# Performance work log

Measured on AMD Instinct MI355X. Metric: run time of the kernel, lower is better.

Reference implementation:

```python
import jax, jax.numpy as jnp
import numpy as np

NS = 4  # ns_mesh hard-coded to [4,4,4] in the original forward


def _interp_weights(positions, cell):
    """Order-3 (M3) B-spline interpolation weights and periodic mesh indices.

    Returns w27 (N,27) combined weights and lin (N,27) flat mesh indices.
    """
    frac = positions @ jnp.linalg.inv(cell)          # fractional coords (N,3)
    u = frac * NS
    nearest = jnp.floor(u + 0.5)
    x = u - nearest                                   # in [-0.5, 0.5]
    # order-3 assignment weights at offsets -1, 0, +1
    w = jnp.stack([0.5 * (0.5 - x) ** 2,
                   0.75 - x ** 2,
                   0.5 * (0.5 + x) ** 2], axis=-1)    # (N,3dims,3offs)
    offs = jnp.array([-1, 0, 1], dtype=jnp.int32)
    idx = (nearest[..., None].astype(jnp.int32) + offs) % NS  # (N,3,3)
    w27 = (w[:, 0, :, None, None] * w[:, 1, None, :, None] * w[:, 2, None, None, :]
           ).reshape(-1, 27)
    lin = (idx[:, 0, :, None, None] * NS * NS
           + idx[:, 1, None, :, None] * NS
           + idx[:, 2, None, None, :]).reshape(-1, 27)
    return w27, lin


def _kspace_filter(cell, sigma2):
    """Smeared-Coulomb kernel exp(-k^2 sigma2/2)/k^2 on the rfft half-grid."""
    G = 2.0 * jnp.pi * jnp.linalg.inv(cell).T         # reciprocal lattice rows
    fx = jnp.fft.fftfreq(NS) * NS                     # integer frequencies
    fz = jnp.fft.rfftfreq(NS) * NS
    kvec = (fx[:, None, None, None] * G[0]
            + fx[None, :, None, None] * G[1]
            + fz[None, None, :, None] * G[2])         # (NS,NS,NS//2+1,3)
    k2 = jnp.sum(kvec ** 2, axis=-1)
    k2_safe = jnp.where(k2 > 0, k2, 1.0)
    return jnp.where(k2 > 0, jnp.exp(-k2 * sigma2 * 0.5) / k2_safe, 0.0)


def reference(positions, cell, charges, sigma2, W1, b1, W2, b2, W3, b3):
    w27, lin = _interp_weights(positions, cell)       # (N,27) each
    C = charges.shape[1]
    # points_to_mesh: scatter-add charges with stencil weights
    contrib = (w27[:, :, None] * charges[:, None, :]).reshape(-1, C)
    mesh_flat = jnp.zeros((NS ** 3, C), charges.dtype).at[lin.reshape(-1)].add(contrib)
    mesh = mesh_flat.T.reshape(C, NS, NS, NS)
    # k-space filter: rfft (backward norm) -> multiply -> irfft (forward norm)
    kernel = _kspace_filter(cell, sigma2)
    mesh_hat = jnp.fft.rfftn(mesh, axes=(1, 2, 3))
    mesh = jnp.fft.irfftn(mesh_hat * kernel, s=(NS, NS, NS), axes=(1, 2, 3),
                          norm="forward")
    # mesh_to_points: gather with the same stencil weights
    mesh_flat = mesh.reshape(C, -1).T                 # (NS^3, C)
    pot = jnp.sum(mesh_flat[lin] * w27[:, :, None], axis=1)  # (N,C)
    # tiny MLP on [charge, potential]
    x = jnp.concatenate([charges, pot], axis=1)       # (N,2)
    x = jnp.tanh(x @ W1 + b1)
    x = jnp.tanh(x @ W2 + b2)
    return jnp.sum(x @ W3 + b3)


def setup_inputs() -> dict:
    key = jax.random.key(0)
    ks = jax.random.split(key, 8)
    N = 2_000_000
    L = 6.0
    positions = jax.random.uniform(ks[0], (N, 3), dtype=jnp.float32) * L
    cell = jnp.eye(3, dtype=jnp.float32) * L
    charges = jax.random.normal(ks[1], (N, 1), dtype=jnp.float32)
    sigma2 = jnp.asarray(1.0, dtype=jnp.float32)
    s1, s2, s3 = (1.0 / np.sqrt(2), 1.0 / np.sqrt(10), 1.0 / np.sqrt(10))
    W1 = jax.random.normal(ks[2], (2, 10), jnp.float32) * s1
    b1 = jnp.zeros((10,), jnp.float32)
    W2 = jax.random.normal(ks[3], (10, 10), jnp.float32) * s2
    b2 = jnp.zeros((10,), jnp.float32)
    W3 = jax.random.normal(ks[4], (10, 1), jnp.float32) * s3
    b3 = jnp.zeros((1,), jnp.float32)
    return {"positions": positions, "cell": cell, "charges": charges,
            "sigma2": sigma2, "W1": W1, "b1": b1, "W2": W2, "b2": b2,
            "W3": W3, "b3": b3}
```

## Files before the change

### kernel.cpp

```cpp
#include <hip/hip_runtime.h>
#include <math.h>

#define NSM 4
#define NCELL 64
#define R1_BLOCKS 64

typedef float f32x2 __attribute__((ext_vector_type(2)));


__device__ __forceinline__ f32x2 splat2(float s) { f32x2 v; v.x = s; v.y = s; return v; }

__device__ __forceinline__ f32x2 pkfma(f32x2 a, f32x2 b, f32x2 c) {
#if __has_builtin(__builtin_elementwise_fma)
    return __builtin_elementwise_fma(a, b, c);
#else
    f32x2 r; r.x = fmaf(a.x, b.x, c.x); r.y = fmaf(a.y, b.y, c.y); return r;
#endif
}

__device__ __forceinline__ void inv3x3(const float* __restrict__ C, float* inv) {
    float a=C[0],b=C[1],c=C[2],d=C[3],e=C[4],f=C[5],g=C[6],h=C[7],i=C[8];
    float A  =  (e*i - f*h);
    float B  = -(d*i - f*g);
    float Cc =  (d*h - e*g);
    float det = a*A + b*B + c*Cc;
    float rd = 1.0f/det;
    inv[0] = A*rd;        inv[1] = (c*h - b*i)*rd; inv[2] = (b*f - c*e)*rd;
    inv[3] = B*rd;        inv[4] = (a*i - c*g)*rd; inv[5] = (c*d - a*f)*rd;
    inv[6] = Cc*rd;       inv[7] = (b*g - a*h)*rd; inv[8] = (a*e - b*d)*rd;
}

struct AxW { float wm, w0, wp; int n; };
__device__ __forceinline__ AxW axw(float u) {
    AxW r;
    float nf = rintf(u);
    float x  = u - nf;
    r.w0 = 0.75f - x*x;
    float tm = 0.5f - x;  r.wm = 0.5f*tm*tm;
    float tp = 0.5f + x;  r.wp = 0.5f*tp*tp;
    r.n = ((int)nf) & 3;
    return r;
}

__device__ __forceinline__ void axis_w4(float u, float* __restrict__ W) {
    AxW a = axw(u);
    #pragma unroll
    for (int j = 0; j < 4; j++) {
        float w = (a.n == j)         ? a.w0 : 0.0f;
        w       = (a.n == ((j+1)&3)) ? a.wm : w;
        w       = (a.n == ((j+3)&3)) ? a.wp : w;
        W[j] = w;
    }
}

__device__ __forceinline__ float tanh1(float x) {
    float e = __expf(x + x);
    return fmaf(-2.0f, __builtin_amdgcn_rcpf(e + 1.0f), 1.0f);
}
__device__ __forceinline__ f32x2 tanh2v(f32x2 v) {
    float e0 = __expf(v.x + v.x);
    float e1 = __expf(v.y + v.y);
    f32x2 r;
    r.x = fmaf(-2.0f, __builtin_amdgcn_rcpf(e0 + 1.0f), 1.0f);
    r.y = fmaf(-2.0f, __builtin_amdgcn_rcpf(e1 + 1.0f), 1.0f);
    return r;
}


__device__ __forceinline__ void scatter_one(float px, float py, float pz, float q,
                                            const float* __restrict__ ci,
                                            f32x2* __restrict__ macc) {
    float fx = px*ci[0] + py*ci[3] + pz*ci[6];
    float fy = px*ci[1] + py*ci[4] + pz*ci[7];
    float fz = px*ci[2] + py*ci[5] + pz*ci[8];
    float X[4], Y[4], Z[4];
    axis_w4(fx*(float)NSM, X);
    axis_w4(fy*(float)NSM, Y);
    axis_w4(fz*(float)NSM, Z);
    f32x2 z01; z01.x = Z[0]; z01.y = Z[1];
    f32x2 z23; z23.x = Z[2]; z23.y = Z[3];
    float qX[4];
    #pragma unroll
    for (int x = 0; x < 4; x++) qX[x] = q * X[x];
    #pragma unroll
    for (int x = 0; x < 4; x++) {
        #pragma unroll
        for (int y = 0; y < 4; y++) {
            f32x2 w2 = splat2(qX[x] * Y[y]);
            macc[x*8 + y*2    ] = pkfma(w2, z01, macc[x*8 + y*2    ]);
            macc[x*8 + y*2 + 1] = pkfma(w2, z23, macc[x*8 + y*2 + 1]);
        }
    }
}

__global__ __launch_bounds__(256) void scatter_kernel(
        const float* __restrict__ pos, const float* __restrict__ cell,
        const float* __restrict__ charges, float* __restrict__ partial, int N) {
    __shared__ f32x2 red[128][32];
    __shared__ f32x2 red2[8][32];
    float ci[9]; inv3x3(cell, ci);

    f32x2 macc[32];
    #pragma unroll
    for (int c = 0; c < 32; c++) macc[c] = splat2(0.0f);

    const float4* posv = (const float4*)pos;
    const float4* qv   = (const float4*)charges;
    long b = (long)blockIdx.x * blockDim.x + threadIdx.x;
    long i = b * 4;
    if (i + 3 < N) {
        float4 p0 = posv[3*b], p1 = posv[3*b+1], p2 = posv[3*b+2];
        float4 q4 = qv[b];
        scatter_one(p0.x, p0.y, p0.z, q4.x, ci, macc);
        scatter_one(p0.w, p1.x, p1.y, q4.y, ci, macc);
        scatter_one(p1.z, p1.w, p2.x, q4.z, ci, macc);
        scatter_one(p2.y, p2.z, p2.w, q4.w, ci, macc);
    } else if (i < N) {
        for (long k = i; k < N; k++)
            scatter_one(pos[3*k], pos[3*k+1], pos[3*k+2], charges[k], ci, macc);
    }

    #pragma unroll
    for (int c = 0; c < 32; c++) {
        macc[c].x += __shfl_xor(macc[c].x, 32);
        macc[c].y += __shfl_xor(macc[c].y, 32);
    }
    int t = threadIdx.x;
    int row = (t >> 6) * 32 + (t & 31);
    if ((t & 32) == 0) {
        int sw = t & 31;
        #pragma unroll
        for (int c = 0; c < 32; c++) red[row][c ^ sw] = macc[c];
    }
    __syncthreads();
    int p = t & 31, g = t >> 5;
    f32x2 sum = splat2(0.0f);
    #pragma unroll
    for (int i2 = 0; i2 < 16; i2++) {
        int r = g*16 + i2;
        sum += red[r][p ^ (r & 31)];
    }
    red2[g][p] = sum;
    __syncthreads();
    if (t < NCELL) {
        const float* r2 = (const float*)&red2[0][0];
        int pair = t >> 1, comp = t & 1;
        float s = 0.0f;
        #pragma unroll
        for (int gg = 0; gg < 8; gg++) s += r2[(gg*32 + pair)*2 + comp];
        partial[(long)blockIdx.x * NCELL + t] = s;
    }
}


__global__ __launch_bounds__(256) void reduce_stage1_kernel(
        const float* __restrict__ partial, int nb, float* __restrict__ partial2) {
    __shared__ float acc[4][64];
    int t = threadIdx.x;
    int c = t & 63, g = t >> 6;
    float s = 0.0f;
    for (int r = blockIdx.x + 64*g; r < nb; r += 256)
        s += partial[(long)r * NCELL + c];
    acc[g][c] = s;
    __syncthreads();
    if (t < 64) {
        float v = ((acc[0][t] + acc[1][t]) + acc[2][t]) + acc[3][t];
        partial2[(long)blockIdx.x * NCELL + t] = v;
    }
}


__global__ __launch_bounds__(256) void reduce_filter_kernel(
        const float* __restrict__ partial2,
        const float* __restrict__ cell, const float* __restrict__ sigma2p,
        float* __restrict__ mesh_out) {
    __shared__ float4 redA[16][16];
    __shared__ float mm[64];
    __shared__ float gr[64];
    int t = threadIdx.x;

    int c4 = t & 15, g = t >> 4;
    float4 v = make_float4(0.f, 0.f, 0.f, 0.f);
    const float4* p4 = (const float4*)partial2;
    for (int b = g; b < R1_BLOCKS; b += 16) {
        float4 x = p4[b*16 + c4];
        v.x += x.x; v.y += x.y; v.z += x.z; v.w += x.w;
    }
    redA[g][c4] = v;
    __syncthreads();
    if (t < 16) {
        float4 tot = make_float4(0.f, 0.f, 0.f, 0.f);
        #pragma unroll
        for (int gg = 0; gg < 16; gg++) {
            float4 x = redA[gg][t];
            tot.x += x.x; tot.y += x.y; tot.z += x.z; tot.w += x.w;
        }
        ((float4*)mm)[t] = tot;
    }
    __syncthreads();

    if (t < 64) {
        float ci[9]; inv3x3(cell, ci);
        float s2 = sigma2p[0];
        const float twopi = 6.2831853071795864769f;
        float G0x = twopi*ci[0], G0y = twopi*ci[3], G0z = twopi*ci[6];
        float G1x = twopi*ci[1], G1y = twopi*ci[4], G1z = twopi*ci[7];
        float G2x = twopi*ci[2], G2y = twopi*ci[5], G2z = twopi*ci[8];
        int dx = t >> 4, dy = (t >> 2) & 3, dz = t & 3;
        float acc = 0.0f;
        for (int a = 0; a < 4; a++) {
            float fa = (a < 2) ? (float)a : (float)(a - 4);
            for (int b = 0; b < 4; b++) {
                float fb = (b < 2) ? (float)b : (float)(b - 4);
                for (int c = 0; c < 4; c++) {
                    if ((a | b | c) == 0) continue;
                    float fc = (c < 2) ? (float)c : (float)(c - 4);
                    float kx = fa*G0x + fb*G1x + fc*G2x;
                    float ky = fa*G0y + fb*G1y + fc*G2y;
                    float kz = fa*G0z + fb*G1z + fc*G2z;
                    float k2 = kx*kx + ky*ky + kz*kz;
                    float K  = expf(-k2 * s2 * 0.5f) / k2;
                    int ph = (a*dx + b*dy + c*dz) & 3;
                    float cs = (ph == 0) ? 1.0f : ((ph == 2) ? -1.0f : 0.0f);
                    acc += K * cs;
                }
            }
        }
        gr[t] = acc;
    }
    __syncthreads();
    if (t < 64) {
        int dx = t >> 4, dy = (t >> 2) & 3, dz = t & 3;
        float o = 0.0f;
        for (int s = 0; s < 64; s++) {
            int sx = s >> 4, sy = (s >> 2) & 3, sz = s & 3;
            int d = ((dx - sx) & 3)*16 + ((dy - sy) & 3)*4 + ((dz - sz) & 3);
            o += gr[d] * mm[s];
        }
        mesh_out[t] = o;
    }
}


__device__ __forceinline__ float pot_one(float px, float py, float pz,
                                         const float* __restrict__ ci,
                                         const float* __restrict__ mpad) {
    float fx = px*ci[0] + py*ci[3] + pz*ci[6];
    float fy = px*ci[1] + py*ci[4] + pz*ci[7];
    float fz = px*ci[2] + py*ci[5] + pz*ci[8];
    AxW X = axw(fx*(float)NSM);
    AxW Y = axw(fy*(float)NSM);
    AxW Z = axw(fz*(float)NSM);
    int base = X.n*36 + Y.n*6 + Z.n;
    float yacc[3];
    #pragma unroll
    for (int a = 0; a < 3; a++) {
        float zc0, zc1, zc2;
        {
            const float* r = &mpad[base + a*36];
            zc0 = Z.wm*r[0];  zc0 = fmaf(Z.w0, r[1], zc0);  zc0 = fmaf(Z.wp, r[2], zc0);
            zc1 = Z.wm*r[6];  zc1 = fmaf(Z.w0, r[7], zc1);  zc1 = fmaf(Z.wp, r[8], zc1);
            zc2 = Z.wm*r[12]; zc2 = fmaf(Z.w0, r[13], zc2); zc2 = fmaf(Z.wp, r[14], zc2);
        }
        float s = Y.wm*zc0;
        s = fmaf(Y.w0, zc1, s);
        s = fmaf(Y.wp, zc2, s);
        yacc[a] = s;
    }
    float pot = X.wm*yacc[0];
    pot = fmaf(X.w0, yacc[1], pot);
    pot = fmaf(X.wp, yacc[2], pot);
    return pot;
}

__global__ __launch_bounds__(256) void gather_mlp_kernel(
        const float* __restrict__ pos, const float* __restrict__ cell,
        const float* __restrict__ charges,
        const float* __restrict__ W1, const float* __restrict__ b1,
        const float* __restrict__ W2, const float* __restrict__ b2,
        const float* __restrict__ W3, const float* __restrict__ b3,
        const float* __restrict__ meshf, float* __restrict__ bsum, int N) {
    __shared__ float mpad[216];
    __shared__ float wavesum[4];
    if (threadIdx.x < 216) {
        int i = threadIdx.x / 36, rem = threadIdx.x % 36;
        int j = rem / 6, k = rem % 6;
        mpad[threadIdx.x] = meshf[((i+3)&3)*16 + ((j+3)&3)*4 + ((k+3)&3)];
    }
    float ci[9]; inv3x3(cell, ci);

    float w1r0[10], w1r1[10], b1r[10], w2r[10][10], b2r[10], w3r[10];
    #pragma unroll
    for (int j = 0; j < 10; j++) {
        w1r0[j] = W1[j]; w1r1[j] = W1[10 + j];
        b1r[j] = b1[j];  b2r[j] = b2[j]; w3r[j] = W3[j];
    }
    #pragma unroll
    for (int i = 0; i < 10; i++) {
        #pragma unroll
        for (int j = 0; j < 10; j++) w2r[i][j] = W2[10*i + j];
    }
    float b3r = b3[0];
    __syncthreads();

    long t4 = (long)blockIdx.x * blockDim.x + threadIdx.x;
    long i0 = t4 * 4;
    float ysum = 0.0f;

    if (i0 + 3 < N) {
        const float4* posv = (const float4*)pos;
        float4 p0 = posv[3*t4], p1 = posv[3*t4+1], p2 = posv[3*t4+2];
        float4 q4 = ((const float4*)charges)[t4];

        float pt0 = pot_one(p0.x, p0.y, p0.z, ci, mpad);
        float pt1 = pot_one(p0.w, p1.x, p1.y, ci, mpad);
        float pt2 = pot_one(p1.z, p1.w, p2.x, ci, mpad);
        float pt3 = pot_one(p2.y, p2.z, p2.w, ci, mpad);

        f32x2 q01; q01.x = q4.x; q01.y = q4.y;
        f32x2 q23; q23.x = q4.z; q23.y = q4.w;
        f32x2 pA;  pA.x = pt0;  pA.y = pt1;
        f32x2 pB;  pB.x = pt2;  pB.y = pt3;

        f32x2 h1a[10], h1b[10];
        #pragma unroll
        for (int j = 0; j < 10; j++) {
            f32x2 ta = pkfma(pA, splat2(w1r1[j]), splat2(b1r[j]));
            ta = pkfma(q01, splat2(w1r0[j]), ta);
            h1a[j] = tanh2v(ta);
            f32x2 tb = pkfma(pB, splat2(w1r1[j]), splat2(b1r[j]));
            tb = pkfma(q23, splat2(w1r0[j]), tb);
            h1b[j] = tanh2v(tb);
        }
        f32x2 h2a[10], h2b[10];
        #pragma unroll
        for (int j = 0; j < 10; j++) {
            f32x2 aa = splat2(b2r[j]), ab = splat2(b2r[j]);
            #pragma unroll
            for (int i = 0; i < 10; i++) {
                f32x2 w = splat2(w2r[i][j]);
                aa = pkfma(h1a[i], w, aa);
                ab = pkfma(h1b[i], w, ab);
            }
            h2a[j] = tanh2v(aa);
            h2b[j] = tanh2v(ab);
        }
        f32x2 ya = splat2(b3r), yb = splat2(b3r);
        #pragma unroll
        for (int j = 0; j < 10; j++) {
            f32x2 w = splat2(w3r[j]);
            ya = pkfma(h2a[j], w, ya);
            yb = pkfma(h2b[j], w, yb);
        }
        ysum = ya.x + ya.y + yb.x + yb.y;
    } else if (i0 < N) {
        for (long k = i0; k < N; k++) {
            float pt = pot_one(pos[3*k], pos[3*k+1], pos[3*k+2], ci, mpad);
            float q  = charges[k];
            float h1[10], h2[10];
            #pragma unroll
            for (int j = 0; j < 10; j++)
                h1[j] = tanh1(fmaf(q, w1r0[j], fmaf(pt, w1r1[j], b1r[j])));
            #pragma unroll
            for (int j = 0; j < 10; j++) {
                float acc = b2r[j];
                #pragma unroll
                for (int i = 0; i < 10; i++) acc = fmaf(h1[i], w2r[i][j], acc);
                h2[j] = tanh1(acc);
            }
            float y = b3r;
            #pragma unroll
            for (int j = 0; j < 10; j++) y = fmaf(h2[j], w3r[j], y);
            ysum += y;
        }
    }

    ysum += __shfl_down(ysum, 32);
    ysum += __shfl_down(ysum, 16);
    ysum += __shfl_down(ysum, 8);
    ysum += __shfl_down(ysum, 4);
    ysum += __shfl_down(ysum, 2);
    ysum += __shfl_down(ysum, 1);
    int wid  = threadIdx.x >> 6;
    int lane = threadIdx.x & 63;
    if (lane == 0) wavesum[wid] = ysum;
    __syncthreads();
    if (threadIdx.x == 0)
        bsum[blockIdx.x] = wavesum[0] + wavesum[1] + wavesum[2] + wavesum[3];
}


__global__ __launch_bounds__(256) void final_sum_kernel(
        const float* __restrict__ bsum, int nb, float* __restrict__ out) {
    __shared__ float wavesum[4];
    float s = 0.0f;
    for (int i = threadIdx.x; i < nb; i += 256) s += bsum[i];
    s += __shfl_down(s, 32);
    s += __shfl_down(s, 16);
    s += __shfl_down(s, 8);
    s += __shfl_down(s, 4);
    s += __shfl_down(s, 2);
    s += __shfl_down(s, 1);
    int wid  = threadIdx.x >> 6;
    int lane = threadIdx.x & 63;
    if (lane == 0) wavesum[wid] = s;
    __syncthreads();
    if (threadIdx.x == 0)
        out[0] = wavesum[0] + wavesum[1] + wavesum[2] + wavesum[3];
}


extern "C" void kernel_launch(void* const* d_in, const int* in_sizes, int n_in,
                              void* d_out, int out_size, void* d_ws, size_t ws_size,
                              hipStream_t stream) {
    const float* pos     = (const float*)d_in[0];
    const float* cell    = (const float*)d_in[1];
    const float* charges = (const float*)d_in[2];
    const float* sigma2  = (const float*)d_in[3];
    const float* W1 = (const float*)d_in[4];
    const float* b1 = (const float*)d_in[5];
    const float* W2 = (const float*)d_in[6];
    const float* b2 = (const float*)d_in[7];
    const float* W3 = (const float*)d_in[8];
    const float* b3 = (const float*)d_in[9];
    int N = in_sizes[2];

    int nblocks = (int)(((long)N + 1023) / 1024);

    float* partial  = (float*)d_ws;
    float* partial2 = partial + (long)nblocks * NCELL;
    float* meshf    = partial2 + (long)R1_BLOCKS * NCELL;
    float* bsum     = meshf + NCELL;

    scatter_kernel<<<nblocks, 256, 0, stream>>>(pos, cell, charges, partial, N);
    reduce_stage1_kernel<<<R1_BLOCKS, 256, 0, stream>>>(partial, nblocks, partial2);
    reduce_filter_kernel<<<1, 256, 0, stream>>>(partial2, cell, sigma2, meshf);
    gather_mlp_kernel<<<nblocks, 256, 0, stream>>>(pos, cell, charges,
                                                   W1, b1, W2, b2, W3, b3,
                                                   meshf, bsum, N);
    final_sum_kernel<<<1, 256, 0, stream>>>(bsum, nblocks, (float*)d_out);
}
```

Baseline: 58.18 us.

## Use fixed grid-stride grids and fold filter stage into reduce and gather kernels

Scatter and gather kernels now run a fixed 1024-block grid-stride loop instead of one block per 1024 particles. This shrinks the partial-mesh array that the first reduction reads. The single-block reduce_filter kernel is removed: block 0 of the first reduction computes the Green's-function table, and every gather block redundantly does the final reduction and circular convolution in shared memory. The intent is to drop one serial single-block launch and cut reduction traffic, at the cost of duplicated small work in each gather block and a fixed grid size tied to N.

```diff
diff --git a/kernel.cpp b/kernel.cpp
--- a/kernel.cpp
+++ b/kernel.cpp
@@ -3,6 +3,8 @@
 
 #define NSM 4
 #define NCELL 64
+#define SC_BLOCKS 1024
+#define GA_BLOCKS 1024
 #define R1_BLOCKS 64
 
 typedef float f32x2 __attribute__((ext_vector_type(2)));
@@ -106,18 +108,22 @@
 
     const float4* posv = (const float4*)pos;
     const float4* qv   = (const float4*)charges;
-    long b = (long)blockIdx.x * blockDim.x + threadIdx.x;
-    long i = b * 4;
-    if (i + 3 < N) {
-        float4 p0 = posv[3*b], p1 = posv[3*b+1], p2 = posv[3*b+2];
-        float4 q4 = qv[b];
-        scatter_one(p0.x, p0.y, p0.z, q4.x, ci, macc);
-        scatter_one(p0.w, p1.x, p1.y, q4.y, ci, macc);
-        scatter_one(p1.z, p1.w, p2.x, q4.z, ci, macc);
-        scatter_one(p2.y, p2.z, p2.w, q4.w, ci, macc);
-    } else if (i < N) {
-        for (long k = i; k < N; k++)
-            scatter_one(pos[3*k], pos[3*k+1], pos[3*k+2], charges[k], ci, macc);
+    long NB4    = ((long)N + 3) / 4;
+    long stride = (long)SC_BLOCKS * 256;
+
+    for (long b = (long)blockIdx.x * blockDim.x + threadIdx.x; b < NB4; b += stride) {
+        long i = b * 4;
+        if (i + 3 < N) {
+            float4 p0 = posv[3*b], p1 = posv[3*b+1], p2 = posv[3*b+2];
+            float4 q4 = qv[b];
+            scatter_one(p0.x, p0.y, p0.z, q4.x, ci, macc);
+            scatter_one(p0.w, p1.x, p1.y, q4.y, ci, macc);
+            scatter_one(p1.z, p1.w, p2.x, q4.z, ci, macc);
+            scatter_one(p2.y, p2.z, p2.w, q4.w, ci, macc);
+        } else {
+            for (long k = i; k < N; k++)
+                scatter_one(pos[3*k], pos[3*k+1], pos[3*k+2], charges[k], ci, macc);
+        }
     }
 
     #pragma unroll
@@ -154,52 +160,21 @@
 
 
 __global__ __launch_bounds__(256) void reduce_stage1_kernel(
-        const float* __restrict__ partial, int nb, float* __restrict__ partial2) {
+        const float* __restrict__ partial, float* __restrict__ partial2,
+        const float* __restrict__ cell, const float* __restrict__ sigma2p,
+        float* __restrict__ grbuf) {
     __shared__ float acc[4][64];
     int t = threadIdx.x;
     int c = t & 63, g = t >> 6;
     float s = 0.0f;
-    for (int r = blockIdx.x + 64*g; r < nb; r += 256)
+    #pragma unroll
+    for (int j = 0; j < 4; j++) {
+        int r = blockIdx.x + 64*g + 256*j;
         s += partial[(long)r * NCELL + c];
+    }
     acc[g][c] = s;
-    __syncthreads();
-    if (t < 64) {
-        float v = ((acc[0][t] + acc[1][t]) + acc[2][t]) + acc[3][t];
-        partial2[(long)blockIdx.x * NCELL + t] = v;
-    }
-}
-
-
-__global__ __launch_bounds__(256) void reduce_filter_kernel(
-        const float* __restrict__ partial2,
-        const float* __restrict__ cell, const float* __restrict__ sigma2p,
-        float* __restrict__ mesh_out) {
-    __shared__ float4 redA[16][16];
-    __shared__ float mm[64];
-    __shared__ float gr[64];
-    int t = threadIdx.x;
-
-    int c4 = t & 15, g = t >> 4;
-    float4 v = make_float4(0.f, 0.f, 0.f, 0.f);
-    const float4* p4 = (const float4*)partial2;
-    for (int b = g; b < R1_BLOCKS; b += 16) {
-        float4 x = p4[b*16 + c4];
-        v.x += x.x; v.y += x.y; v.z += x.z; v.w += x.w;
-    }
-    redA[g][c4] = v;
-    __syncthreads();
-    if (t < 16) {
-        float4 tot = make_float4(0.f, 0.f, 0.f, 0.f);
-        #pragma unroll
-        for (int gg = 0; gg < 16; gg++) {
-            float4 x = redA[gg][t];
-            tot.x += x.x; tot.y += x.y; tot.z += x.z; tot.w += x.w;
-        }
-        ((float4*)mm)[t] = tot;
-    }
-    __syncthreads();
-
-    if (t < 64) {
+
+    if (blockIdx.x == 0 && t < 64) {
         float ci[9]; inv3x3(cell, ci);
         float s2 = sigma2p[0];
         const float twopi = 6.2831853071795864769f;
@@ -207,37 +182,32 @@
         float G1x = twopi*ci[1], G1y = twopi*ci[4], G1z = twopi*ci[7];
         float G2x = twopi*ci[2], G2y = twopi*ci[5], G2z = twopi*ci[8];
         int dx = t >> 4, dy = (t >> 2) & 3, dz = t & 3;
-        float acc = 0.0f;
+        float accg = 0.0f;
         for (int a = 0; a < 4; a++) {
             float fa = (a < 2) ? (float)a : (float)(a - 4);
             for (int b = 0; b < 4; b++) {
                 float fb = (b < 2) ? (float)b : (float)(b - 4);
-                for (int c = 0; c < 4; c++) {
-                    if ((a | b | c) == 0) continue;
-                    float fc = (c < 2) ? (float)c : (float)(c - 4);
+                for (int cc = 0; cc < 4; cc++) {
+                    if ((a | b | cc) == 0) continue;
+                    float fc = (cc < 2) ? (float)cc : (float)(cc - 4);
                     float kx = fa*G0x + fb*G1x + fc*G2x;
                     float ky = fa*G0y + fb*G1y + fc*G2y;
                     float kz = fa*G0z + fb*G1z + fc*G2z;
                     float k2 = kx*kx + ky*ky + kz*kz;
                     float K  = expf(-k2 * s2 * 0.5f) / k2;
-                    int ph = (a*dx + b*dy + c*dz) & 3;
+                    int ph = (a*dx + b*dy + cc*dz) & 3;
                     float cs = (ph == 0) ? 1.0f : ((ph == 2) ? -1.0f : 0.0f);
-                    acc += K * cs;
+                    accg += K * cs;
                 }
             }
         }
-        gr[t] = acc;
-    }
+        grbuf[t] = accg;
+    }
+
     __syncthreads();
     if (t < 64) {
-        int dx = t >> 4, dy = (t >> 2) & 3, dz = t & 3;
-        float o = 0.0f;
-        for (int s = 0; s < 64; s++) {
-            int sx = s >> 4, sy = (s >> 2) & 3, sz = s & 3;
-            int d = ((dx - sx) & 3)*16 + ((dy - sy) & 3)*4 + ((dz - sz) & 3);
-            o += gr[d] * mm[s];
-        }
-        mesh_out[t] = o;
+        float v = ((acc[0][t] + acc[1][t]) + acc[2][t]) + acc[3][t];
+        partial2[(long)blockIdx.x * NCELL + t] = v;
     }
 }
 
@@ -279,13 +249,51 @@
         const float* __restrict__ W1, const float* __restrict__ b1,
         const float* __restrict__ W2, const float* __restrict__ b2,
         const float* __restrict__ W3, const float* __restrict__ b3,
-        const float* __restrict__ meshf, float* __restrict__ bsum, int N) {
+        const float* __restrict__ partial2, const float* __restrict__ grbuf,
+        float* __restrict__ bsum, int N) {
+    __shared__ float acc[4][64];
+    __shared__ float mm[64];
+    __shared__ float grl[64];
+    __shared__ float mfl[64];
     __shared__ float mpad[216];
     __shared__ float wavesum[4];
-    if (threadIdx.x < 216) {
-        int i = threadIdx.x / 36, rem = threadIdx.x % 36;
+    int t = threadIdx.x;
+    int c = t & 63, g = t >> 6;
+
+    {
+        float s = 0.0f;
+        #pragma unroll
+        for (int j = 0; j < 16; j++) {
+            int r = g + 4*j;
+            s += partial2[(long)r * NCELL + c];
+        }
+        acc[g][c] = s;
+        if (t < 64) grl[t] = grbuf[t];
+    }
+    __syncthreads();
+    if (t < 64) mm[t] = ((acc[0][t] + acc[1][t]) + acc[2][t]) + acc[3][t];
+    __syncthreads();
+
+    {
+        int cx = c >> 4, cy = (c >> 2) & 3, cz = c & 3;
+        int dxrow = ((cx - g) & 3) * 16;
+        float o = 0.0f;
+        #pragma unroll
+        for (int k = 0; k < 16; k++) {
+            int sy = k >> 2, sz = k & 3;
+            int d = dxrow + ((cy - sy) & 3)*4 + ((cz - sz) & 3);
+            o = fmaf(grl[d], mm[g*16 + k], o);
+        }
+        acc[g][c] = o;
+    }
+    __syncthreads();
+    if (t < 64) mfl[t] = ((acc[0][t] + acc[1][t]) + acc[2][t]) + acc[3][t];
+    __syncthreads();
+
+    if (t < 216) {
+        int i = t / 36, rem = t % 36;
         int j = rem / 6, k = rem % 6;
-        mpad[threadIdx.x] = meshf[((i+3)&3)*16 + ((j+3)&3)*4 + ((k+3)&3)];
+        mpad[t] = mfl[((i+3)&3)*16 + ((j+3)&3)*4 + ((k+3)&3)];
     }
     float ci[9]; inv3x3(cell, ci);
 
@@ -303,75 +311,78 @@
     float b3r = b3[0];
     __syncthreads();
 
-    long t4 = (long)blockIdx.x * blockDim.x + threadIdx.x;
-    long i0 = t4 * 4;
+    long NB4    = ((long)N + 3) / 4;
+    long stride = (long)GA_BLOCKS * 256;
     float ysum = 0.0f;
 
-    if (i0 + 3 < N) {
-        const float4* posv = (const float4*)pos;
-        float4 p0 = posv[3*t4], p1 = posv[3*t4+1], p2 = posv[3*t4+2];
-        float4 q4 = ((const float4*)charges)[t4];
-
-        float pt0 = pot_one(p0.x, p0.y, p0.z, ci, mpad);
-        float pt1 = pot_one(p0.w, p1.x, p1.y, ci, mpad);
-        float pt2 = pot_one(p1.z, p1.w, p2.x, ci, mpad);
-        float pt3 = pot_one(p2.y, p2.z, p2.w, ci, mpad);
-
-        f32x2 q01; q01.x = q4.x; q01.y = q4.y;
-        f32x2 q23; q23.x = q4.z; q23.y = q4.w;
-        f32x2 pA;  pA.x = pt0;  pA.y = pt1;
-        f32x2 pB;  pB.x = pt2;  pB.y = pt3;
-
-        f32x2 h1a[10], h1b[10];
-        #pragma unroll
-        for (int j = 0; j < 10; j++) {
-            f32x2 ta = pkfma(pA, splat2(w1r1[j]), splat2(b1r[j]));
-            ta = pkfma(q01, splat2(w1r0[j]), ta);
-            h1a[j] = tanh2v(ta);
-            f32x2 tb = pkfma(pB, splat2(w1r1[j]), splat2(b1r[j]));
-            tb = pkfma(q23, splat2(w1r0[j]), tb);
-            h1b[j] = tanh2v(tb);
-        }
-        f32x2 h2a[10], h2b[10];
-        #pragma unroll
-        for (int j = 0; j < 10; j++) {
-            f32x2 aa = splat2(b2r[j]), ab = splat2(b2r[j]);
-            #pragma unroll
-            for (int i = 0; i < 10; i++) {
-                f32x2 w = splat2(w2r[i][j]);
-                aa = pkfma(h1a[i], w, aa);
-                ab = pkfma(h1b[i], w, ab);
-            }
-            h2a[j] = tanh2v(aa);
-            h2b[j] = tanh2v(ab);
-        }
-        f32x2 ya = splat2(b3r), yb = splat2(b3r);
-        #pragma unroll
-        for (int j = 0; j < 10; j++) {
-            f32x2 w = splat2(w3r[j]);
-            ya = pkfma(h2a[j], w, ya);
-            yb = pkfma(h2b[j], w, yb);
-        }
-        ysum = ya.x + ya.y + yb.x + yb.y;
-    } else if (i0 < N) {
-        for (long k = i0; k < N; k++) {
-            float pt = pot_one(pos[3*k], pos[3*k+1], pos[3*k+2], ci, mpad);
-            float q  = charges[k];
-            float h1[10], h2[10];
-            #pragma unroll
-            for (int j = 0; j < 10; j++)
-                h1[j] = tanh1(fmaf(q, w1r0[j], fmaf(pt, w1r1[j], b1r[j])));
+    for (long b = (long)blockIdx.x * blockDim.x + threadIdx.x; b < NB4; b += stride) {
+        long i0 = b * 4;
+        if (i0 + 3 < N) {
+            const float4* posv = (const float4*)pos;
+            float4 p0 = posv[3*b], p1 = posv[3*b+1], p2 = posv[3*b+2];
+            float4 q4 = ((const float4*)charges)[b];
+
+            float pt0 = pot_one(p0.x, p0.y, p0.z, ci, mpad);
+            float pt1 = pot_one(p0.w, p1.x, p1.y, ci, mpad);
+            float pt2 = pot_one(p1.z, p1.w, p2.x, ci, mpad);
+            float pt3 = pot_one(p2.y, p2.z, p2.w, ci, mpad);
+
+            f32x2 q01; q01.x = q4.x; q01.y = q4.y;
+            f32x2 q23; q23.x = q4.z; q23.y = q4.w;
+            f32x2 pA;  pA.x = pt0;  pA.y = pt1;
+            f32x2 pB;  pB.x = pt2;  pB.y = pt3;
+
+            f32x2 h1a[10], h1b[10];
             #pragma unroll
             for (int j = 0; j < 10; j++) {
-                float acc = b2r[j];
+                f32x2 ta = pkfma(pA, splat2(w1r1[j]), splat2(b1r[j]));
+                ta = pkfma(q01, splat2(w1r0[j]), ta);
+                h1a[j] = tanh2v(ta);
+                f32x2 tb = pkfma(pB, splat2(w1r1[j]), splat2(b1r[j]));
+                tb = pkfma(q23, splat2(w1r0[j]), tb);
+                h1b[j] = tanh2v(tb);
+            }
+            f32x2 h2a[10], h2b[10];
+            #pragma unroll
+            for (int j = 0; j < 10; j++) {
+                f32x2 aa = splat2(b2r[j]), ab = splat2(b2r[j]);
                 #pragma unroll
-                for (int i = 0; i < 10; i++) acc = fmaf(h1[i], w2r[i][j], acc);
-                h2[j] = tanh1(acc);
+                for (int i = 0; i < 10; i++) {
+                    f32x2 w = splat2(w2r[i][j]);
+                    aa = pkfma(h1a[i], w, aa);
+                    ab = pkfma(h1b[i], w, ab);
+                }
+                h2a[j] = tanh2v(aa);
+                h2b[j] = tanh2v(ab);
             }
-            float y = b3r;
+            f32x2 ya = splat2(b3r), yb = splat2(b3r);
             #pragma unroll
-            for (int j = 0; j < 10; j++) y = fmaf(h2[j], w3r[j], y);
-            ysum += y;
+            for (int j = 0; j < 10; j++) {
+                f32x2 w = splat2(w3r[j]);
+                ya = pkfma(h2a[j], w, ya);
+                yb = pkfma(h2b[j], w, yb);
+            }
+            ysum += ya.x + ya.y + yb.x + yb.y;
+        } else {
+            for (long k = i0; k < N; k++) {
+                float pt = pot_one(pos[3*k], pos[3*k+1], pos[3*k+2], ci, mpad);
+                float q  = charges[k];
+                float h1[10], h2[10];
+                #pragma unroll
+                for (int j = 0; j < 10; j++)
+                    h1[j] = tanh1(fmaf(q, w1r0[j], fmaf(pt, w1r1[j], b1r[j])));
+                #pragma unroll
+                for (int j = 0; j < 10; j++) {
+                    float a2 = b2r[j];
+                    #pragma unroll
+                    for (int i = 0; i < 10; i++) a2 = fmaf(h1[i], w2r[i][j], a2);
+                    h2[j] = tanh1(a2);
+                }
+                float y = b3r;
+                #pragma unroll
+                for (int j = 0; j < 10; j++) y = fmaf(h2[j], w3r[j], y);
+                ysum += y;
+            }
         }
     }
 
@@ -381,11 +392,11 @@
     ysum += __shfl_down(ysum, 4);
     ysum += __shfl_down(ysum, 2);
     ysum += __shfl_down(ysum, 1);
-    int wid  = threadIdx.x >> 6;
-    int lane = threadIdx.x & 63;
+    int wid  = t >> 6;
+    int lane = t & 63;
     if (lane == 0) wavesum[wid] = ysum;
     __syncthreads();
-    if (threadIdx.x == 0)
+    if (t == 0)
         bsum[blockIdx.x] = wavesum[0] + wavesum[1] + wavesum[2] + wavesum[3];
 }
 
@@ -425,18 +436,16 @@
     const float* b3 = (const float*)d_in[9];
     int N = in_sizes[2];
 
-    int nblocks = (int)(((long)N + 1023) / 1024);
-
     float* partial  = (float*)d_ws;
-    float* partial2 = partial + (long)nblocks * NCELL;
-    float* meshf    = partial2 + (long)R1_BLOCKS * NCELL;
-    float* bsum     = meshf + NCELL;
-
-    scatter_kernel<<<nblocks, 256, 0, stream>>>(pos, cell, charges, partial, N);
-    reduce_stage1_kernel<<<R1_BLOCKS, 256, 0, stream>>>(partial, nblocks, partial2);
-    reduce_filter_kernel<<<1, 256, 0, stream>>>(partial2, cell, sigma2, meshf);
-    gather_mlp_kernel<<<nblocks, 256, 0, stream>>>(pos, cell, charges,
-                                                   W1, b1, W2, b2, W3, b3,
-                                                   meshf, bsum, N);
-    final_sum_kernel<<<1, 256, 0, stream>>>(bsum, nblocks, (float*)d_out);
-}
+    float* partial2 = partial + (long)SC_BLOCKS * NCELL;
+    float* grbuf    = partial2 + (long)R1_BLOCKS * NCELL;
+    float* bsum     = grbuf + NCELL;
+
+    scatter_kernel<<<SC_BLOCKS, 256, 0, stream>>>(pos, cell, charges, partial, N);
+    reduce_stage1_kernel<<<R1_BLOCKS, 256, 0, stream>>>(partial, partial2,
+                                                        cell, sigma2, grbuf);
+    gather_mlp_kernel<<<GA_BLOCKS, 256, 0, stream>>>(pos, cell, charges,
+                                                     W1, b1, W2, b2, W3, b3,
+                                                     partial2, grbuf, bsum, N);
+    final_sum_kernel<<<1, 256, 0, stream>>>(bsum, GA_BLOCKS, (float*)d_out);
+}
```

After: 59.96 us. 3.1% more time.
